# Kernel optimization log

Hardware: AMD Instinct MI355X
Metric: run time of the kernel (lower is better)

Reference implementation:

```python
import jax, jax.numpy as jnp
import numpy as np

SEQ_LEN, BATCH, INPUT, HIDDEN, N_OUT = 512, 128, 512, 1024, 4


def setup_inputs() -> dict:
    key = jax.random.key(0)
    ks = jax.random.split(key, 8)
    s_ih = 1.0 / np.sqrt(HIDDEN)
    inp = {
        "inputs": jax.random.normal(ks[0], (SEQ_LEN, BATCH, INPUT), dtype=jnp.float32),
        "h0": jnp.zeros((BATCH, HIDDEN), dtype=jnp.float32),
        "c0": jnp.zeros((BATCH, HIDDEN), dtype=jnp.float32),
        # PyTorch LSTMCell params: weight_ih [4H, I], weight_hh [4H, H], biases [4H]
        "W_ih": jax.random.uniform(ks[1], (4 * HIDDEN, INPUT), jnp.float32, -s_ih, s_ih),
        "W_hh": jax.random.uniform(ks[2], (4 * HIDDEN, HIDDEN), jnp.float32, -s_ih, s_ih),
        "b_ih": jax.random.uniform(ks[3], (4 * HIDDEN,), jnp.float32, -s_ih, s_ih),
        "b_hh": jax.random.uniform(ks[4], (4 * HIDDEN,), jnp.float32, -s_ih, s_ih),
        "W_dec": jax.random.uniform(ks[5], (N_OUT, HIDDEN), jnp.float32, -s_ih, s_ih),
        "b_dec": jax.random.uniform(ks[6], (N_OUT,), jnp.float32, -s_ih, s_ih),
    }
    return inp


def reference(inputs, h0, c0, W_ih, W_hh, b_ih, b_hh, W_dec, b_dec):
    # Precompute input projections for all timesteps in one big GEMM:
    # [S, B, I] @ [I, 4H] -> [S, B, 4H]
    x_proj = jnp.einsum('sbi,gi->sbg', inputs, W_ih) + b_ih + b_hh

    def step(carry, xp):
        h, c = carry
        gates = xp + h @ W_hh.T  # [B, 4H]
        i, f, g, o = jnp.split(gates, 4, axis=-1)  # PyTorch gate order i,f,g,o
        i = jax.nn.sigmoid(i)
        f = jax.nn.sigmoid(f)
        g = jnp.tanh(g)
        o = jax.nn.sigmoid(o)
        c_new = f * c + i * g
        h_new = o * jnp.tanh(c_new)
        return (h_new, c_new), None

    (h_last, _), _ = jax.lax.scan(step, (h0, c0), x_proj)
    logits = h_last @ W_dec.T + b_dec  # [B, 4]
    # Original applies nn.Softmax(dim=0), i.e. over the batch dimension.
    return jax.nn.softmax(logits, axis=0)
```

## Files before the change

kernel.cpp:

```cpp
#include <hip/hip_runtime.h>
#include <math.h>

#define SEQ   512
#define BATCH 128
#define INP   512
#define HID   1024
#define G4    4096
#define NOUT  4

typedef short bf16x8 __attribute__((ext_vector_type(8)));
typedef float f32x4  __attribute__((ext_vector_type(4)));

__device__ __forceinline__ unsigned short f2bf(float x) {
  unsigned int u = __float_as_uint(x);
  unsigned int r = (u + 0x7FFFu + ((u >> 16) & 1u)) >> 16;
  return (unsigned short)r;
}
__device__ __forceinline__ float bf2f(unsigned short h) {
  return __uint_as_float(((unsigned int)h) << 16);
}

__device__ __forceinline__ bf16x8 ld_h16_uc(const unsigned short* p) {
  union { unsigned long long q[2]; bf16x8 v; } u;
  unsigned long long* pp = (unsigned long long*)(void*)p;
  u.q[0] = __hip_atomic_load(pp,     __ATOMIC_RELAXED, __HIP_MEMORY_SCOPE_SYSTEM);
  u.q[1] = __hip_atomic_load(pp + 1, __ATOMIC_RELAXED, __HIP_MEMORY_SCOPE_SYSTEM);
  return u.v;
}

__global__ void prepack_w(const float* __restrict__ W,
                          unsigned short* __restrict__ Whi,
                          unsigned short* __restrict__ Wlo) {
  int T = blockIdx.x * blockDim.x + threadIdx.x;
  int L = T & 63;
  int kstep = (T >> 6) & 31;
  int bk = T >> 11;
  int m = L & 15, q = L >> 4;
  int row = (m & 3) * HID + bk * 4 + (m >> 2);
  int k = kstep * 32 + q * 8;
  const float* src = W + (size_t)row * HID + k;
  size_t o = (size_t)T * 8;
#pragma unroll
  for (int i = 0; i < 8; i++) {
    float x = src[i];
    unsigned short h = f2bf(x);
    Whi[o + i] = h;
    Wlo[o + i] = f2bf(x - bf2f(h));
  }
}

__global__ void init_state(const float* __restrict__ h0, const float* __restrict__ c0,
                           unsigned short* __restrict__ hhi, unsigned short* __restrict__ hlo,
                           float* __restrict__ cT, unsigned int* __restrict__ flags) {
  int idx = blockIdx.x * blockDim.x + threadIdx.x;
  if (idx < 1024) flags[idx] = 0u;
  int b = idx >> 10;
  int j = idx & (HID - 1);
  float x = h0[idx];
  unsigned short h = f2bf(x);
  hhi[idx] = h;
  hlo[idx] = f2bf(x - bf2f(h));
  cT[j * BATCH + b] = c0[idx];
}

__global__ void transpose_in(const float* __restrict__ in, float* __restrict__ xt,
                             int nrows) {
  __shared__ float s[32][33];
  int tx = threadIdx.x & 31, ty = threadIdx.x >> 5;
  int n0 = blockIdx.x * 32, i0 = blockIdx.y * 32;
#pragma unroll
  for (int r = 0; r < 4; r++) {
    int n = n0 + ty + 8 * r;
    s[ty + 8 * r][tx] = in[(size_t)n * INP + i0 + tx];
  }
  __syncthreads();
#pragma unroll
  for (int r = 0; r < 4; r++) {
    int i = i0 + ty + 8 * r;
    xt[(size_t)i * nrows + n0 + tx] = s[tx][ty + 8 * r];
  }
}

__global__ __launch_bounds__(256, 3)
void gemm_xproj(const float* __restrict__ A, const float* __restrict__ Bm,
                const float* __restrict__ b_ih, const float* __restrict__ b_hh,
                float* __restrict__ C, int N) {
  __shared__ float As[32][128];
  __shared__ float Bs[32][128];
  int t = threadIdx.x;
  int g0 = blockIdx.x * 128;
  int n0 = blockIdx.y * 128;
  int mg = (t >> 4) * 8, nn = (t & 15) * 8;
  float acc[8][8] = {};
  for (int k0 = 0; k0 < INP; k0 += 32) {
#pragma unroll
    for (int r = 0; r < 4; r++) {
      int idx = t + 256 * r;
      int g = idx >> 3, i4 = idx & 7;
      float4 v = *(const float4*)&A[(size_t)(g0 + g) * INP + k0 + 4 * i4];
      As[4 * i4 + 0][g] = v.x; As[4 * i4 + 1][g] = v.y;
      As[4 * i4 + 2][g] = v.z; As[4 * i4 + 3][g] = v.w;
    }
#pragma unroll
    for (int r = 0; r < 4; r++) {
      int idx = t + 256 * r;
      int kk = idx >> 5, n4 = idx & 31;
      *(float4*)&Bs[kk][4 * n4] = *(const float4*)&Bm[(size_t)(k0 + kk) * N + n0 + 4 * n4];
    }
    __syncthreads();
#pragma unroll 4
    for (int kk = 0; kk < 32; kk++) {
      float4 a0 = *(const float4*)&As[kk][mg];
      float4 a1 = *(const float4*)&As[kk][mg + 4];
      float4 bb0 = *(const float4*)&Bs[kk][nn];
      float4 bb1 = *(const float4*)&Bs[kk][nn + 4];
      float av[8] = {a0.x, a0.y, a0.z, a0.w, a1.x, a1.y, a1.z, a1.w};
      float bv[8] = {bb0.x, bb0.y, bb0.z, bb0.w, bb1.x, bb1.y, bb1.z, bb1.w};
#pragma unroll
      for (int i2 = 0; i2 < 8; i2++)
#pragma unroll
        for (int j2 = 0; j2 < 8; j2++)
          acc[i2][j2] = fmaf(av[i2], bv[j2], acc[i2][j2]);
    }
    __syncthreads();
  }
#pragma unroll
  for (int i2 = 0; i2 < 8; i2++) {
    int g = g0 + mg + i2;
    float bias = b_ih[g] + b_hh[g];
#pragma unroll
    for (int j2 = 0; j2 < 8; j2++) {
      C[(size_t)g * N + n0 + nn + j2] = acc[i2][j2] + bias;
    }
  }
}

__global__ __launch_bounds__(256)
void lstm_seq(const unsigned short* __restrict__ Whi,
              const unsigned short* __restrict__ Wlo,
              const float* __restrict__ XP, int N, int CT, int step0,
              unsigned short* __restrict__ h0hi, unsigned short* __restrict__ h0lo,
              unsigned short* __restrict__ h1hi, unsigned short* __restrict__ h1lo,
              float* __restrict__ cT, unsigned int* flags) {
  __shared__ bf16x8 Wlds[8192];
  __shared__ unsigned short hstage[64][2][12];

  int bk = blockIdx.x;
  int jblk = bk >> 1;
  int bh2 = bk & 1;
  int t = threadIdx.x;
  int w = t >> 6;
  int L = t & 63;
  int n = L & 15, q = L >> 4;
  int b = bh2 * 64 + w * 16 + n;
  int j0 = jblk * 8 + q;

  {
    float4* ldsf = (float4*)Wlds;
    const float4* s1 = (const float4*)(Whi + (size_t)jblk * 32768);
    const float4* s2 = (const float4*)(Wlo + (size_t)jblk * 32768);
#pragma unroll
    for (int i = 0; i < 16; i++) ldsf[t + 256 * i] = s1[t + 256 * i];
#pragma unroll
    for (int i = 0; i < 16; i++) ldsf[4096 + t + 256 * i] = s2[t + 256 * i];
  }

  int ci0 = j0 * BATCH + b;
  int ci1 = (j0 + 4) * BATCH + b;
  float cc0 = cT[ci0];
  float cc1 = cT[ci1];

  size_t hoff = (size_t)b * HID + q * 8;

  int r_bl   = t >> 2;
  int r_arr  = (t >> 1) & 1;
  int r_half = t & 1;
  size_t r_off = (size_t)(bh2 * 64 + r_bl) * HID + jblk * 8 + r_half * 4;

  __syncthreads();

  float xa0[4], xa1[4];
#pragma unroll
  for (int g = 0; g < 4; g++) {
    xa0[g] = XP[(size_t)(g * HID + j0) * N + b];
    xa1[g] = XP[(size_t)(g * HID + j0 + 4) * N + b];
  }

  for (int tt = 0; tt < CT; tt++) {
    int gs = step0 + tt;
    int odd = gs & 1;
    const unsigned short* Bh = (odd ? h1hi : h0hi) + hoff;
    const unsigned short* Bl = (odd ? h1lo : h0lo) + hoff;
    unsigned short* dhi = odd ? h0hi : h1hi;
    unsigned short* dlo = odd ? h0lo : h1lo;

    f32x4 acc0 = {0.f, 0.f, 0.f, 0.f};
    f32x4 acc1 = {0.f, 0.f, 0.f, 0.f};
#pragma unroll 8
    for (int ks = 0; ks < 32; ks++) {
      bf16x8 bhv = ld_h16_uc(Bh + ks * 32);
      bf16x8 blv = ld_h16_uc(Bl + ks * 32);
      bf16x8 ah0 = Wlds[ks * 64 + L];
      bf16x8 ah1 = Wlds[2048 + ks * 64 + L];
      bf16x8 al0 = Wlds[4096 + ks * 64 + L];
      bf16x8 al1 = Wlds[6144 + ks * 64 + L];
      acc0 = __builtin_amdgcn_mfma_f32_16x16x32_bf16(ah0, bhv, acc0, 0, 0, 0);
      acc1 = __builtin_amdgcn_mfma_f32_16x16x32_bf16(ah1, bhv, acc1, 0, 0, 0);
      acc0 = __builtin_amdgcn_mfma_f32_16x16x32_bf16(ah0, blv, acc0, 0, 0, 0);
      acc1 = __builtin_amdgcn_mfma_f32_16x16x32_bf16(ah1, blv, acc1, 0, 0, 0);
      acc0 = __builtin_amdgcn_mfma_f32_16x16x32_bf16(al0, bhv, acc0, 0, 0, 0);
      acc1 = __builtin_amdgcn_mfma_f32_16x16x32_bf16(al1, bhv, acc1, 0, 0, 0);
    }

    {
      float i_ = 1.f / (1.f + expf(-(acc0[0] + xa0[0])));
      float f_ = 1.f / (1.f + expf(-(acc0[1] + xa0[1])));
      float g_ = tanhf(acc0[2] + xa0[2]);
      float o_ = 1.f / (1.f + expf(-(acc0[3] + xa0[3])));
      cc0 = f_ * cc0 + i_ * g_;
      float hn = o_ * tanhf(cc0);
      unsigned short hh = f2bf(hn);
      hstage[w * 16 + n][0][q] = hh;
      hstage[w * 16 + n][1][q] = f2bf(hn - bf2f(hh));
    }
    {
      float i_ = 1.f / (1.f + expf(-(acc1[0] + xa1[0])));
      float f_ = 1.f / (1.f + expf(-(acc1[1] + xa1[1])));
      float g_ = tanhf(acc1[2] + xa1[2]);
      float o_ = 1.f / (1.f + expf(-(acc1[3] + xa1[3])));
      cc1 = f_ * cc1 + i_ * g_;
      float hn = o_ * tanhf(cc1);
      unsigned short hh = f2bf(hn);
      hstage[w * 16 + n][0][q + 4] = hh;
      hstage[w * 16 + n][1][q + 4] = f2bf(hn - bf2f(hh));
    }

    __syncthreads();

    {
      unsigned long long v =
          *(const unsigned long long*)&hstage[r_bl][r_arr][r_half * 4];
      unsigned short* basep = r_arr ? dlo : dhi;
      __hip_atomic_store((unsigned long long*)(void*)(basep + r_off), v,
                         __ATOMIC_RELAXED, __HIP_MEMORY_SCOPE_SYSTEM);
    }

    float xb0[4], xb1[4];
    {
      int tpf = (tt + 1 < CT) ? (tt + 1) : tt;
      const float* xpc = XP + (size_t)tpf * BATCH;
#pragma unroll
      for (int g = 0; g < 4; g++) {
        xb0[g] = xpc[(size_t)(g * HID + j0) * N + b];
        xb1[g] = xpc[(size_t)(g * HID + j0 + 4) * N + b];
      }
    }

    unsigned tgt = (unsigned)(gs + 1);
    __syncthreads();
    if (t == 0)
      __hip_atomic_store(&flags[bk], tgt, __ATOMIC_RELAXED,
                         __HIP_MEMORY_SCOPE_SYSTEM);
    if (bk == 0) {
      unsigned gcnt = 0;
      while (__hip_atomic_load(&flags[t], __ATOMIC_RELAXED,
                               __HIP_MEMORY_SCOPE_SYSTEM) < tgt &&
             ++gcnt < (1u << 16))
        __builtin_amdgcn_s_sleep(1);
      __syncthreads();
      if (t < 8)
        __hip_atomic_store(&flags[512 + t * 32], tgt, __ATOMIC_RELAXED,
                           __HIP_MEMORY_SCOPE_SYSTEM);
    } else if (t == 0) {
      unsigned gcnt = 0;
      const unsigned int* gop = &flags[512 + (bk & 7) * 32];
      while (__hip_atomic_load(gop, __ATOMIC_RELAXED,
                               __HIP_MEMORY_SCOPE_SYSTEM) < tgt &&
             ++gcnt < (1u << 16))
        __builtin_amdgcn_s_sleep(1);
    }
    __syncthreads();

#pragma unroll
    for (int g = 0; g < 4; g++) { xa0[g] = xb0[g]; xa1[g] = xb1[g]; }
  }

  cT[ci0] = cc0;
  cT[ci1] = cc1;
}

__global__ void decode_softmax(const unsigned short* __restrict__ hhi,
                               const unsigned short* __restrict__ hlo,
                               const float* __restrict__ Wd,
                               const float* __restrict__ bd, float* __restrict__ out) {
  __shared__ float lg[NOUT][BATCH];
  __shared__ float mx[NOUT], sm[NOUT];
  int t = threadIdx.x;
  int b = t >> 2, o = t & 3;
  float s = bd[o];
  for (int j = 0; j < HID; j++) {
    float hv = bf2f(hhi[(size_t)b * HID + j]) + bf2f(hlo[(size_t)b * HID + j]);
    s += hv * Wd[o * HID + j];
  }
  lg[o][b] = s;
  __syncthreads();
  if (t < NOUT) {
    float m = -1e30f;
    for (int b2 = 0; b2 < BATCH; b2++) m = fmaxf(m, lg[t][b2]);
    float ss = 0.f;
    for (int b2 = 0; b2 < BATCH; b2++) ss += expf(lg[t][b2] - m);
    mx[t] = m; sm[t] = ss;
  }
  __syncthreads();
  out[b * NOUT + o] = expf(lg[o][b] - mx[o]) / sm[o];
}

extern "C" void kernel_launch(void* const* d_in, const int* in_sizes, int n_in,
                              void* d_out, int out_size, void* d_ws, size_t ws_size,
                              hipStream_t stream) {
  const float* inputs = (const float*)d_in[0];
  const float* h0     = (const float*)d_in[1];
  const float* c0     = (const float*)d_in[2];
  const float* W_ih   = (const float*)d_in[3];
  const float* W_hh   = (const float*)d_in[4];
  const float* b_ih   = (const float*)d_in[5];
  const float* b_hh   = (const float*)d_in[6];
  const float* W_dec  = (const float*)d_in[7];
  const float* b_dec  = (const float*)d_in[8];
  float* out = (float*)d_out;

  char* w = (char*)d_ws;
  unsigned short* Whi = (unsigned short*)w;  w += (size_t)G4 * HID * 2;
  unsigned short* Wlo = (unsigned short*)w;  w += (size_t)G4 * HID * 2;
  unsigned short* hhi[2], *hlo[2];
  hhi[0] = (unsigned short*)w;  w += (size_t)BATCH * HID * 2;
  hhi[1] = (unsigned short*)w;  w += (size_t)BATCH * HID * 2;
  hlo[0] = (unsigned short*)w;  w += (size_t)BATCH * HID * 2;
  hlo[1] = (unsigned short*)w;  w += (size_t)BATCH * HID * 2;
  float* cT = (float*)w;        w += (size_t)HID * BATCH * 4;
  unsigned int* flags = (unsigned int*)w;  w += 4096;
  size_t used = (size_t)(w - (char*)d_ws);

  size_t per_ct = ((size_t)INP * BATCH + (size_t)G4 * BATCH) * 4;
  int CT = 1;
  if (ws_size > used) {
    size_t avail = (ws_size - used) / per_ct;
    for (int c = SEQ; c >= 1; c >>= 1)
      if ((size_t)c <= avail) { CT = c; break; }
  }
  float* Xt = (float*)w;  w += (size_t)INP * BATCH * CT * 4;
  float* XP = (float*)w;
  int N = CT * BATCH;

  prepack_w<<<(256 * 32 * 64) / 256, 256, 0, stream>>>(W_hh, Whi, Wlo);
  init_state<<<BATCH * HID / 256, 256, 0, stream>>>(h0, c0, hhi[0], hlo[0], cT, flags);

  for (int t0 = 0; t0 < SEQ; t0 += CT) {
    transpose_in<<<dim3(N / 32, INP / 32), 256, 0, stream>>>(
        inputs + (size_t)t0 * BATCH * INP, Xt, N);
    gemm_xproj<<<dim3(G4 / 128, N / 128), 256, 0, stream>>>(
        W_ih, Xt, b_ih, b_hh, XP, N);

    int Nv = N, CTv = CT, step0 = t0;
    void* kargs[] = {
        (void*)&Whi, (void*)&Wlo, (void*)&XP, (void*)&Nv, (void*)&CTv,
        (void*)&step0, (void*)&hhi[0], (void*)&hlo[0], (void*)&hhi[1],
        (void*)&hlo[1], (void*)&cT, (void*)&flags};
    hipLaunchCooperativeKernel((const void*)lstm_seq, dim3(256), dim3(256),
                               kargs, 0, stream);
  }

  decode_softmax<<<1, 512, 0, stream>>>(hhi[0], hlo[0], W_dec, b_dec, out);
}
```

Measured before the change: 12.50 ms.

## Split recurrent LSTM step across 512 blocks with 4 hidden units each

Each persistent block of the cooperative LSTM kernel now owns 4 hidden units instead of 8. This halves its LDS weight slice and its MFMA chain per timestep, and doubles the grid to 512 blocks so two can share a CU. The grid barrier is widened to poll 512 arrival flags and fan out through 16 release flags. The intent is to shorten the per-step critical path and overlap latency across co-resident blocks. In exchange it doubles global reads of h per step and makes the barrier costlier, and it adds a non-cooperative launch fallback that could deadlock if all blocks are not resident.

Result: slower. 19.79 ms (+58.4%).

```diff
diff --git a/kernel.cpp b/kernel.cpp
--- a/kernel.cpp
+++ b/kernel.cpp
@@ -53,7 +53,7 @@
                            unsigned short* __restrict__ hhi, unsigned short* __restrict__ hlo,
                            float* __restrict__ cT, unsigned int* __restrict__ flags) {
   int idx = blockIdx.x * blockDim.x + threadIdx.x;
-  if (idx < 1024) flags[idx] = 0u;
+  if (idx < 2048) flags[idx] = 0u;
   int b = idx >> 10;
   int j = idx & (HID - 1);
   float x = h0[idx];
@@ -142,49 +142,44 @@
               unsigned short* __restrict__ h0hi, unsigned short* __restrict__ h0lo,
               unsigned short* __restrict__ h1hi, unsigned short* __restrict__ h1lo,
               float* __restrict__ cT, unsigned int* flags) {
-  __shared__ bf16x8 Wlds[8192];
+  __shared__ bf16x8 Wlds[4096];
   __shared__ unsigned short hstage[64][2][12];
 
   int bk = blockIdx.x;
-  int jblk = bk >> 1;
+  int sblk = bk >> 1;
   int bh2 = bk & 1;
   int t = threadIdx.x;
   int w = t >> 6;
   int L = t & 63;
   int n = L & 15, q = L >> 4;
   int b = bh2 * 64 + w * 16 + n;
-  int j0 = jblk * 8 + q;
+  int j0 = sblk * 4 + q;
 
   {
     float4* ldsf = (float4*)Wlds;
-    const float4* s1 = (const float4*)(Whi + (size_t)jblk * 32768);
-    const float4* s2 = (const float4*)(Wlo + (size_t)jblk * 32768);
-#pragma unroll
-    for (int i = 0; i < 16; i++) ldsf[t + 256 * i] = s1[t + 256 * i];
-#pragma unroll
-    for (int i = 0; i < 16; i++) ldsf[4096 + t + 256 * i] = s2[t + 256 * i];
+    const float4* s1 = (const float4*)(Whi + (size_t)sblk * 16384);
+    const float4* s2 = (const float4*)(Wlo + (size_t)sblk * 16384);
+#pragma unroll
+    for (int i = 0; i < 8; i++) ldsf[t + 256 * i] = s1[t + 256 * i];
+#pragma unroll
+    for (int i = 0; i < 8; i++) ldsf[2048 + t + 256 * i] = s2[t + 256 * i];
   }
 
   int ci0 = j0 * BATCH + b;
-  int ci1 = (j0 + 4) * BATCH + b;
   float cc0 = cT[ci0];
-  float cc1 = cT[ci1];
 
   size_t hoff = (size_t)b * HID + q * 8;
 
-  int r_bl   = t >> 2;
-  int r_arr  = (t >> 1) & 1;
-  int r_half = t & 1;
-  size_t r_off = (size_t)(bh2 * 64 + r_bl) * HID + jblk * 8 + r_half * 4;
+  int r_bl  = t >> 1;
+  int r_arr = t & 1;
+  size_t r_off = (size_t)(bh2 * 64 + r_bl) * HID + sblk * 4;
 
   __syncthreads();
 
-  float xa0[4], xa1[4];
-#pragma unroll
-  for (int g = 0; g < 4; g++) {
+  float xa0[4];
+#pragma unroll
+  for (int g = 0; g < 4; g++)
     xa0[g] = XP[(size_t)(g * HID + j0) * N + b];
-    xa1[g] = XP[(size_t)(g * HID + j0 + 4) * N + b];
-  }
 
   for (int tt = 0; tt < CT; tt++) {
     int gs = step0 + tt;
@@ -195,21 +190,15 @@
     unsigned short* dlo = odd ? h0lo : h1lo;
 
     f32x4 acc0 = {0.f, 0.f, 0.f, 0.f};
-    f32x4 acc1 = {0.f, 0.f, 0.f, 0.f};
 #pragma unroll 8
     for (int ks = 0; ks < 32; ks++) {
       bf16x8 bhv = ld_h16_uc(Bh + ks * 32);
       bf16x8 blv = ld_h16_uc(Bl + ks * 32);
       bf16x8 ah0 = Wlds[ks * 64 + L];
-      bf16x8 ah1 = Wlds[2048 + ks * 64 + L];
-      bf16x8 al0 = Wlds[4096 + ks * 64 + L];
-      bf16x8 al1 = Wlds[6144 + ks * 64 + L];
+      bf16x8 al0 = Wlds[2048 + ks * 64 + L];
       acc0 = __builtin_amdgcn_mfma_f32_16x16x32_bf16(ah0, bhv, acc0, 0, 0, 0);
-      acc1 = __builtin_amdgcn_mfma_f32_16x16x32_bf16(ah1, bhv, acc1, 0, 0, 0);
       acc0 = __builtin_amdgcn_mfma_f32_16x16x32_bf16(ah0, blv, acc0, 0, 0, 0);
-      acc1 = __builtin_amdgcn_mfma_f32_16x16x32_bf16(ah1, blv, acc1, 0, 0, 0);
       acc0 = __builtin_amdgcn_mfma_f32_16x16x32_bf16(al0, bhv, acc0, 0, 0, 0);
-      acc1 = __builtin_amdgcn_mfma_f32_16x16x32_bf16(al1, bhv, acc1, 0, 0, 0);
     }
 
     {
@@ -223,37 +212,24 @@
       hstage[w * 16 + n][0][q] = hh;
       hstage[w * 16 + n][1][q] = f2bf(hn - bf2f(hh));
     }
-    {
-      float i_ = 1.f / (1.f + expf(-(acc1[0] + xa1[0])));
-      float f_ = 1.f / (1.f + expf(-(acc1[1] + xa1[1])));
-      float g_ = tanhf(acc1[2] + xa1[2]);
-      float o_ = 1.f / (1.f + expf(-(acc1[3] + xa1[3])));
-      cc1 = f_ * cc1 + i_ * g_;
-      float hn = o_ * tanhf(cc1);
-      unsigned short hh = f2bf(hn);
-      hstage[w * 16 + n][0][q + 4] = hh;
-      hstage[w * 16 + n][1][q + 4] = f2bf(hn - bf2f(hh));
-    }
-
-    __syncthreads();
-
-    {
+
+    __syncthreads();
+
+    if (t < 128) {
       unsigned long long v =
-          *(const unsigned long long*)&hstage[r_bl][r_arr][r_half * 4];
+          *(const unsigned long long*)&hstage[r_bl][r_arr][0];
       unsigned short* basep = r_arr ? dlo : dhi;
       __hip_atomic_store((unsigned long long*)(void*)(basep + r_off), v,
                          __ATOMIC_RELAXED, __HIP_MEMORY_SCOPE_SYSTEM);
     }
 
-    float xb0[4], xb1[4];
+    float xb0[4];
     {
       int tpf = (tt + 1 < CT) ? (tt + 1) : tt;
       const float* xpc = XP + (size_t)tpf * BATCH;
 #pragma unroll
-      for (int g = 0; g < 4; g++) {
+      for (int g = 0; g < 4; g++)
         xb0[g] = xpc[(size_t)(g * HID + j0) * N + b];
-        xb1[g] = xpc[(size_t)(g * HID + j0 + 4) * N + b];
-      }
     }
 
     unsigned tgt = (unsigned)(gs + 1);
@@ -263,17 +239,19 @@
                          __HIP_MEMORY_SCOPE_SYSTEM);
     if (bk == 0) {
       unsigned gcnt = 0;
-      while (__hip_atomic_load(&flags[t], __ATOMIC_RELAXED,
-                               __HIP_MEMORY_SCOPE_SYSTEM) < tgt &&
+      while ((__hip_atomic_load(&flags[t], __ATOMIC_RELAXED,
+                                __HIP_MEMORY_SCOPE_SYSTEM) < tgt ||
+              __hip_atomic_load(&flags[t + 256], __ATOMIC_RELAXED,
+                                __HIP_MEMORY_SCOPE_SYSTEM) < tgt) &&
              ++gcnt < (1u << 16))
         __builtin_amdgcn_s_sleep(1);
       __syncthreads();
-      if (t < 8)
-        __hip_atomic_store(&flags[512 + t * 32], tgt, __ATOMIC_RELAXED,
+      if (t < 16)
+        __hip_atomic_store(&flags[768 + t * 32], tgt, __ATOMIC_RELAXED,
                            __HIP_MEMORY_SCOPE_SYSTEM);
     } else if (t == 0) {
       unsigned gcnt = 0;
-      const unsigned int* gop = &flags[512 + (bk & 7) * 32];
+      const unsigned int* gop = &flags[768 + (bk & 15) * 32];
       while (__hip_atomic_load(gop, __ATOMIC_RELAXED,
                                __HIP_MEMORY_SCOPE_SYSTEM) < tgt &&
              ++gcnt < (1u << 16))
@@ -282,11 +260,10 @@
     __syncthreads();
 
 #pragma unroll
-    for (int g = 0; g < 4; g++) { xa0[g] = xb0[g]; xa1[g] = xb1[g]; }
+    for (int g = 0; g < 4; g++) xa0[g] = xb0[g];
   }
 
   cT[ci0] = cc0;
-  cT[ci1] = cc1;
 }
 
 __global__ void decode_softmax(const unsigned short* __restrict__ hhi,
@@ -338,7 +315,7 @@
   hlo[0] = (unsigned short*)w;  w += (size_t)BATCH * HID * 2;
   hlo[1] = (unsigned short*)w;  w += (size_t)BATCH * HID * 2;
   float* cT = (float*)w;        w += (size_t)HID * BATCH * 4;
-  unsigned int* flags = (unsigned int*)w;  w += 4096;
+  unsigned int* flags = (unsigned int*)w;  w += 8192;
   size_t used = (size_t)(w - (char*)d_ws);
 
   size_t per_ct = ((size_t)INP * BATCH + (size_t)G4 * BATCH) * 4;
@@ -366,8 +343,12 @@
         (void*)&Whi, (void*)&Wlo, (void*)&XP, (void*)&Nv, (void*)&CTv,
         (void*)&step0, (void*)&hhi[0], (void*)&hlo[0], (void*)&hhi[1],
         (void*)&hlo[1], (void*)&cT, (void*)&flags};
-    hipLaunchCooperativeKernel((const void*)lstm_seq, dim3(256), dim3(256),
-                               kargs, 0, stream);
+    hipError_t ce = hipLaunchCooperativeKernel((const void*)lstm_seq, dim3(512),
+                                               dim3(256), kargs, 0, stream);
+    if (ce != hipSuccess) {
+      lstm_seq<<<512, 256, 0, stream>>>(Whi, Wlo, XP, Nv, CTv, step0,
+                                        hhi[0], hlo[0], hhi[1], hlo[1], cT, flags);
+    }
   }
 
   decode_softmax<<<1, 512, 0, stream>>>(hhi[0], hlo[0], W_dec, b_dec, out);
```
